# Performance work log

Hardware: AMD Instinct MI355X
Metric: run time of the kernel (lower is better)

The kernel has to match this reference:

```python
import jax, jax.numpy as jnp
import numpy as np

NUM_HEADS = 32
NUM_KV_HEADS = 8
HEAD_DIM = 96
ROPE_BASE = 10000.0


def setup_inputs() -> dict:
    key = jax.random.key(0)
    k1, k2, k3 = jax.random.split(key, 3)
    B, S, H = 2, 2048, 3072
    op_size = NUM_HEADS * HEAD_DIM + 2 * NUM_KV_HEADS * HEAD_DIM  # 4608
    hidden_states = jax.random.normal(k1, (B, S, H), dtype=jnp.float32)
    w_qkv = jax.random.normal(k2, (op_size, H), dtype=jnp.float32) * (H ** -0.5)
    w_o = jax.random.normal(k3, (H, H), dtype=jnp.float32) * (H ** -0.5)
    position_ids = jnp.broadcast_to(jnp.arange(S, dtype=jnp.int64), (B, S))
    return {"hidden_states": hidden_states, "position_ids": position_ids,
            "w_qkv": w_qkv, "w_o": w_o}


def _rotate_half(x):
    x1, x2 = jnp.split(x, 2, axis=-1)
    return jnp.concatenate((-x2, x1), axis=-1)


def reference(hidden_states, position_ids, w_qkv, w_o):
    B, S, H = hidden_states.shape
    nh, nkv, hd = NUM_HEADS, NUM_KV_HEADS, HEAD_DIM
    n_rep = nh // nkv

    # fused QKV projection (torch Linear: x @ W^T)
    qkv = jnp.einsum('bsh,oh->bso', hidden_states, w_qkv)
    q_pos = nh * hd
    q = qkv[..., :q_pos].reshape(B, S, nh, hd).transpose(0, 2, 1, 3)
    k = qkv[..., q_pos:q_pos + nkv * hd].reshape(B, S, nkv, hd).transpose(0, 2, 1, 3)
    v = qkv[..., q_pos + nkv * hd:].reshape(B, S, nkv, hd).transpose(0, 2, 1, 3)

    # rotary embedding (Phi3RotaryEmbedding, rope_scaling=None)
    inv_freq = 1.0 / (ROPE_BASE ** (jnp.arange(0, hd, 2, dtype=jnp.float32) / hd))
    freqs = position_ids.astype(jnp.float32)[:, :, None] * inv_freq[None, None, :]  # [B,S,hd/2]
    emb = jnp.concatenate((freqs, freqs), axis=-1)  # [B,S,hd]
    cos = jnp.cos(emb)[:, None, :, :]  # unsqueeze head dim
    sin = jnp.sin(emb)[:, None, :, :]
    q = q * cos + _rotate_half(q) * sin
    k = k * cos + _rotate_half(k) * sin

    # repeat_kv: (B, nkv, S, hd) -> (B, nh, S, hd)
    k = jnp.repeat(k, n_rep, axis=1)
    v = jnp.repeat(v, n_rep, axis=1)

    # causal SDPA
    scale = 1.0 / jnp.sqrt(jnp.float32(hd))
    scores = jnp.einsum('bhqd,bhkd->bhqk', q, k) * scale
    causal = jnp.tril(jnp.ones((S, S), dtype=bool))
    scores = jnp.where(causal[None, None], scores, jnp.finfo(scores.dtype).min)
    probs = jax.nn.softmax(scores, axis=-1)
    attn = jnp.einsum('bhqk,bhkd->bhqd', probs, v)  # [B,nh,S,hd]

    attn = attn.transpose(0, 2, 1, 3).reshape(B, S, nh * hd)
    return jnp.einsum('bsh,oh->bso', attn, w_o)
```

## Files before the change

kernel.cpp:

```cpp
#include <hip/hip_runtime.h>
#include <stdint.h>
#include <math.h>

#define B_   2
#define S_   2048
#define H_   3072
#define NH   32
#define NKV  8
#define HD   96
#define OPSZ 4608
#define MM   (B_*S_)

typedef __attribute__((ext_vector_type(8))) short short8;
typedef __attribute__((ext_vector_type(4))) float floatx4;

__device__ __forceinline__ short f2bf(float f) {
    union { float f; uint32_t u; } v; v.f = f;
    uint32_t r = v.u + 0x7fffu + ((v.u >> 16) & 1u);
    return (short)(r >> 16);
}
__device__ __forceinline__ float bf2f(short s) {
    union { uint32_t u; float f; } v; v.u = ((uint32_t)(uint16_t)s) << 16;
    return v.f;
}
__device__ __forceinline__ uint32_t pk_bf_trunc(float lo, float hi) {
    union { float f; uint32_t u; } a, b; a.f = lo; b.f = hi;
    return (a.u >> 16) | (b.u & 0xFFFF0000u);
}
__device__ __forceinline__ float fast_exp2(float x) {
    float r;
    asm volatile("v_exp_f32 %0, %1" : "=v"(r) : "v"(x));
    return r;
}
__device__ __forceinline__ float dpp_max16(float x) {
    union { float f; int i; } a, t;
    a.f = x;
    t.i = __builtin_amdgcn_update_dpp(0, a.i, 0x128, 0xF, 0xF, false); a.f = fmaxf(a.f, t.f);
    t.i = __builtin_amdgcn_update_dpp(0, a.i, 0x124, 0xF, 0xF, false); a.f = fmaxf(a.f, t.f);
    t.i = __builtin_amdgcn_update_dpp(0, a.i, 0x122, 0xF, 0xF, false); a.f = fmaxf(a.f, t.f);
    t.i = __builtin_amdgcn_update_dpp(0, a.i, 0x121, 0xF, 0xF, false); a.f = fmaxf(a.f, t.f);
    return a.f;
}

__device__ __forceinline__ void async_load16(const void* g, void* l) {
    __builtin_amdgcn_global_load_lds(
        (const __attribute__((address_space(1))) void*)g,
        (__attribute__((address_space(3))) void*)l, 16, 0, 0);
}

#define CN1 (MM * H_ / 4)
#define CN2 (OPSZ * H_ / 4)
#define CN3 (H_ * H_ / 4)
__global__ void cast3_f32_bf16(const float* __restrict__ s1, const float* __restrict__ s2,
                               const float* __restrict__ s3, short* __restrict__ d1,
                               short* __restrict__ d2, short* __restrict__ d3) {
    int gid = blockIdx.x * blockDim.x + threadIdx.x;
    int stride = gridDim.x * blockDim.x;
    for (int i = gid; i < CN1; i += stride) {
        float4 v = ((const float4*)s1)[i];
        short4 o; o.x = f2bf(v.x); o.y = f2bf(v.y); o.z = f2bf(v.z); o.w = f2bf(v.w);
        ((short4*)d1)[i] = o;
    }
    for (int i = gid; i < CN2; i += stride) {
        float4 v = ((const float4*)s2)[i];
        short4 o; o.x = f2bf(v.x); o.y = f2bf(v.y); o.z = f2bf(v.z); o.w = f2bf(v.w);
        ((short4*)d2)[i] = o;
    }
    for (int i = gid; i < CN3; i += stride) {
        float4 v = ((const float4*)s3)[i];
        short4 o; o.x = f2bf(v.x); o.y = f2bf(v.y); o.z = f2bf(v.z); o.w = f2bf(v.w);
        ((short4*)d3)[i] = o;
    }
}

template<int OUT_BF16>
__global__ __launch_bounds__(256) void gemm_bt(const short* __restrict__ A, const short* __restrict__ Bm,
                                               float* __restrict__ Cf, short* __restrict__ Cb,
                                               int M, int N, int K) {
    __shared__ short la[2][128 * 32];
    __shared__ short lb[2][128 * 32];
    const int tid  = threadIdx.x;
    const int wave = tid >> 6, lane = tid & 63;
    const int L15  = lane & 15, quad = lane >> 4;

    const int num_n = N >> 7;
    const int linear = blockIdx.x;
    const int group = linear / (8 * num_n);
    const int rem   = linear % (8 * num_n);
    const int m0 = (group * 8 + (rem & 7)) * 128;
    const int n0 = (rem >> 3) * 128;
    const int wm = (wave >> 1) * 64, wn = (wave & 1) * 64;

    const int drow = wave * 32 + (lane >> 2);
    const int dcol = (lane & 3) * 8;
    const short* ga0 = A  + (size_t)(m0 + drow) * K + dcol;
    const short* ga1 = A  + (size_t)(m0 + drow + 16) * K + dcol;
    const short* gb0 = Bm + (size_t)(n0 + drow) * K + dcol;
    const short* gb1 = Bm + (size_t)(n0 + drow + 16) * K + dcol;
    const int lo0 = (wave * 32) * 32, lo1 = (wave * 32 + 16) * 32;

    floatx4 acc[4][4];
    for (int i = 0; i < 4; i++)
        for (int j = 0; j < 4; j++)
            acc[i][j] = (floatx4){0.f, 0.f, 0.f, 0.f};

    auto stage = [&](int k0, int buf) {
        async_load16(ga0 + k0, &la[buf][lo0]);
        async_load16(ga1 + k0, &la[buf][lo1]);
        async_load16(gb0 + k0, &lb[buf][lo0]);
        async_load16(gb1 + k0, &lb[buf][lo1]);
    };

    stage(0, 0);
    const int nk = K >> 5;
    for (int t = 0; t < nk; t++) {
        const int c = t & 1;
        __syncthreads();
        if (t + 1 < nk) stage((t + 1) << 5, 1 - c);

        short8 af[4], bfr[4];
        #pragma unroll
        for (int i = 0; i < 4; i++)
            af[i] = *(const short8*)&la[c][(wm + i * 16 + L15) * 32 + quad * 8];
        #pragma unroll
        for (int j = 0; j < 4; j++)
            bfr[j] = *(const short8*)&lb[c][(wn + j * 16 + L15) * 32 + quad * 8];
        #pragma unroll
        for (int i = 0; i < 4; i++)
            #pragma unroll
            for (int j = 0; j < 4; j++)
                acc[i][j] = __builtin_amdgcn_mfma_f32_16x16x32_bf16(af[i], bfr[j], acc[i][j], 0, 0, 0);
    }

    #pragma unroll
    for (int i = 0; i < 4; i++)
        #pragma unroll
        for (int j = 0; j < 4; j++)
            #pragma unroll
            for (int r = 0; r < 4; r++) {
                int row = m0 + wm + i * 16 + quad * 4 + r;
                int col = n0 + wn + j * 16 + L15;
                float v = acc[i][j][r];
                if (OUT_BF16) Cb[(size_t)row * N + col] = f2bf(v);
                else          Cf[(size_t)row * N + col] = v;
            }
}

__global__ void rope_reorder(const short* __restrict__ qkv, const int* __restrict__ pos_ids,
                             short* __restrict__ Q, short* __restrict__ Kc) {
    const int total = B_ * S_ * (NH + NKV) * HD;
    int idx = blockIdx.x * blockDim.x + threadIdx.x;
    int stride = gridDim.x * blockDim.x;
    for (; idx < total; idx += stride) {
        int d = idx % HD;
        int row = idx / HD;
        int h_all = row % (NH + NKV);
        int sb = row / (NH + NKV);
        int s = sb % S_;
        int b = sb / S_;
        int base = (b * S_ + s) * OPSZ;
        int off = (h_all < NH) ? (h_all * HD + d) : (H_ + (h_all - NH) * HD + d);
        float x = bf2f(qkv[base + off]);
        int delta = (d < 48) ? 48 : -48;
        float x2 = bf2f(qkv[base + off + delta]);
        int fi = d % 48;
        float inv = exp2f((float)fi * -0.2768273412f);
        float theta = (float)pos_ids[b * S_ + s] * inv;
        float sn, cs;
        __sincosf(theta, &sn, &cs);
        float rot = (d < 48) ? -x2 : x2;
        float outv = x * cs + rot * sn;
        if (h_all < NH) {
            outv *= 0.14724438747f;
            Q[((size_t)(b * NH + h_all) * S_ + s) * HD + d] = f2bf(outv);
        } else {
            int kvh = h_all - NH;
            size_t kaddr = ((size_t)(b * NKV + kvh) * S_ + s) * 128
                         + (((d >> 3) + s) & 15) * 8 + (d & 7);
            Kc[kaddr] = f2bf(outv);
        }
    }
}

__global__ __launch_bounds__(256) void v_transpose(const short* __restrict__ qkv, short* __restrict__ Vt) {
    __shared__ short tile[64 * 104];
    int blk = blockIdx.x;
    int st  = blk & 31;
    int kvh = (blk >> 5) & 7;
    int b   = blk >> 8;
    int s0  = st * 64;
    int tid = threadIdx.x;
    #pragma unroll
    for (int i = 0; i < 3; i++) {
        int c = tid + i * 256;
        int row = c / 12, col8 = c % 12;
        *(short8*)&tile[row * 104 + col8 * 8] =
            *(const short8*)(qkv + (size_t)(b * S_ + s0 + row) * OPSZ + 3840 + kvh * HD + col8 * 8);
    }
    __syncthreads();
    #pragma unroll
    for (int i = 0; i < 3; i++) {
        int c = tid + i * 256;
        int d = c >> 3, col8 = c & 7;
        int chunk0 = (col8 - d) & 7;
        short8 v;
        #pragma unroll
        for (int j = 0; j < 8; j++) {
            int col0 = chunk0 * 8 + j;
            int n = ((col0 >> 5) << 1) | (col0 & 1);
            int t = (col0 & 31) >> 1;
            v[j] = tile[(n * 16 + t) * 104 + d];
        }
        *(short8*)(Vt + ((size_t)(b * NKV + kvh) * HD + d) * S_ + s0 + col8 * 8) = v;
    }
}

__global__ __launch_bounds__(256) void flash_attn(const short* __restrict__ Q, const short* __restrict__ Kc,
                                                  const short* __restrict__ Vt, short* __restrict__ attn) {
    __shared__ short kl[2][64 * 128];
    __shared__ short vl[2][112 * 64];
    __shared__ short pl[4][32 * 72];
    const int x = blockIdx.x, h = blockIdx.y, b = blockIdx.z;
    const int kvh = h >> 2;
    const int tid = threadIdx.x, wave = tid >> 6, lane = tid & 63;
    const int L15 = lane & 15, quad = lane >> 4;

    #pragma unroll
    for (int i = 0; i < 2; i++) {
        uint32_t* p = (uint32_t*)&vl[i][96 * 64];
        #pragma unroll
        for (int k = 0; k < 2; k++) {
            int idx = tid + k * 256;
            p[idx] = (idx < 32) ? 0x3F803F80u : 0u;
        }
    }

    const short* kbase = Kc + (size_t)(b * NKV + kvh) * S_ * 128;
    const short* vbase = Vt + (size_t)(b * NKV + kvh) * HD * S_;
    const int klane   = lane * 8;
    const int vrow_lo = lane >> 3;
    const int vcol    = (lane & 7) * 8;

    int rotK[3], rotV[2];
    #pragma unroll
    for (int kk = 0; kk < 3; kk++) rotK[kk] = ((kk * 4 + quad + L15) & 15) * 8;
    #pragma unroll
    for (int kk = 0; kk < 2; kk++) rotV[kk] = ((kk * 4 + quad + L15) & 7) * 8;

    auto stage = [&](int kv0, int buf) {
        const short* ksrc = kbase + (size_t)kv0 * 128;
        #pragma unroll
        for (int i = 0; i < 4; i++) {
            int ck = wave * 4 + i;
            async_load16(ksrc + ck * 512 + klane, &kl[buf][ck * 512]);
        }
        #pragma unroll
        for (int i = 0; i < 3; i++) {
            int ck = wave * 3 + i;
            async_load16(vbase + (size_t)(ck * 8 + vrow_lo) * S_ + kv0 + vcol, &vl[buf][ck * 512]);
        }
    };

    #pragma unroll
    for (int pp = 0; pp < 2; pp++) {
        const int qt = pp ? x : (15 - x);
        const int q0 = qt * 128;
        const int jmax = 2 * qt + 2;

        short8 qf[2][3];
        #pragma unroll
        for (int mm = 0; mm < 2; mm++) {
            const short* qrow = Q + ((size_t)(b * NH + h) * S_ + q0 + wave * 32 + mm * 16 + L15) * HD;
            #pragma unroll
            for (int kk = 0; kk < 3; kk++) qf[mm][kk] = *(const short8*)(qrow + kk * 32 + quad * 8);
        }
        floatx4 o[2][7];
        float m_r[2][4];
        #pragma unroll
        for (int mm = 0; mm < 2; mm++) {
            #pragma unroll
            for (int nn = 0; nn < 7; nn++) o[mm][nn] = (floatx4){0.f, 0.f, 0.f, 0.f};
            #pragma unroll
            for (int r = 0; r < 4; r++) m_r[mm][r] = -3.0e38f;
        }

        __syncthreads();
        stage(0, 0);

        for (int j = 0; j < jmax; j++) {
            const int c = j & 1;
            const int kv0 = j * 64;
            __syncthreads();
            if (j + 1 < jmax) stage(kv0 + 64, 1 - c);

            const short* klp = kl[c];
            const short* vlp = vl[c];

            floatx4 sacc[2][4];
            #pragma unroll
            for (int mm = 0; mm < 2; mm++)
                #pragma unroll
                for (int n = 0; n < 4; n++) sacc[mm][n] = (floatx4){0.f, 0.f, 0.f, 0.f};
            #pragma unroll
            for (int n = 0; n < 4; n++)
                #pragma unroll
                for (int kk = 0; kk < 3; kk++) {
                    short8 kf = *(const short8*)&klp[(n * 16 + L15) * 128 + rotK[kk]];
                    sacc[0][n] = __builtin_amdgcn_mfma_f32_16x16x32_bf16(qf[0][kk], kf, sacc[0][n], 0, 0, 0);
                    sacc[1][n] = __builtin_amdgcn_mfma_f32_16x16x32_bf16(qf[1][kk], kf, sacc[1][n], 0, 0, 0);
                }

            #pragma unroll
            for (int mm = 0; mm < 2; mm++) {
                const int tbase = q0 + wave * 32 + mm * 16;
                if (kv0 + 63 > tbase) {
                    int qr_base = tbase + quad * 4;
                    #pragma unroll
                    for (int n = 0; n < 4; n++) {
                        int kv = kv0 + n * 16 + L15;
                        #pragma unroll
                        for (int r = 0; r < 4; r++)
                            if (kv > qr_base + r) sacc[mm][n][r] = -3.0e38f;
                    }
                }
                float alpha[4];
                #pragma unroll
                for (int r = 0; r < 4; r++) {
                    float mx = fmaxf(fmaxf(sacc[mm][0][r], sacc[mm][1][r]),
                                     fmaxf(sacc[mm][2][r], sacc[mm][3][r]));
                    mx = dpp_max16(mx);
                    float mn = fmaxf(m_r[mm][r], mx);
                    alpha[r] = fast_exp2(m_r[mm][r] - mn);
                    m_r[mm][r] = mn;
                }
                #pragma unroll
                for (int n = 0; n < 4; n++)
                    #pragma unroll
                    for (int r = 0; r < 4; r++)
                        sacc[mm][n][r] = fast_exp2(sacc[mm][n][r] - m_r[mm][r]);
                #pragma unroll
                for (int r = 0; r < 4; r++) {
                    int prow = mm * 16 + quad * 4 + r;
                    *(uint32_t*)&pl[wave][prow * 72 + 2 * L15]      = pk_bf_trunc(sacc[mm][0][r], sacc[mm][1][r]);
                    *(uint32_t*)&pl[wave][prow * 72 + 32 + 2 * L15] = pk_bf_trunc(sacc[mm][2][r], sacc[mm][3][r]);
                }
                #pragma unroll
                for (int nn = 0; nn < 7; nn++)
                    #pragma unroll
                    for (int r = 0; r < 4; r++) o[mm][nn][r] *= alpha[r];
            }

            #pragma unroll
            for (int kk = 0; kk < 2; kk++) {
                short8 af0 = *(const short8*)&pl[wave][L15 * 72 + kk * 32 + quad * 8];
                short8 af1 = *(const short8*)&pl[wave][(16 + L15) * 72 + kk * 32 + quad * 8];
                #pragma unroll
                for (int nn = 0; nn < 7; nn++) {
                    short8 vf = *(const short8*)&vlp[(nn * 16 + L15) * 64 + rotV[kk]];
                    o[0][nn] = __builtin_amdgcn_mfma_f32_16x16x32_bf16(af0, vf, o[0][nn], 0, 0, 0);
                    o[1][nn] = __builtin_amdgcn_mfma_f32_16x16x32_bf16(af1, vf, o[1][nn], 0, 0, 0);
                }
            }
        }

        #pragma unroll
        for (int mm = 0; mm < 2; mm++) {
            float inv_l[4];
            #pragma unroll
            for (int r = 0; r < 4; r++) {
                float l = __shfl(o[mm][6][r], lane & 48);
                inv_l[r] = 1.0f / l;
            }
            #pragma unroll
            for (int nn = 0; nn < 6; nn++)
                #pragma unroll
                for (int r = 0; r < 4; r++) {
                    float v = o[mm][nn][r] * inv_l[r];
                    int row = q0 + wave * 32 + mm * 16 + quad * 4 + r;
                    attn[((size_t)(b * S_) + row) * H_ + h * HD + nn * 16 + L15] = f2bf(v);
                }
        }
    }
}

extern "C" void kernel_launch(void* const* d_in, const int* in_sizes, int n_in,
                              void* d_out, int out_size, void* d_ws, size_t ws_size,
                              hipStream_t stream) {
    const float* hid  = (const float*)d_in[0];
    const int*   pos  = (const int*)d_in[1];
    const float* wqkv = (const float*)d_in[2];
    const float* wo   = (const float*)d_in[3];
    float* out = (float*)d_out;
    char* ws = (char*)d_ws;

    short* hid_b  = (short*)(ws + 0L);
    short* wqkv_b = (short*)(ws + 25165824L);
    short* wo_b   = (short*)(ws + 53477376L);
    short* qkv_b  = (short*)(ws + 72351744L);
    short* q_b    = (short*)(ws + 110100480L);
    short* k_b    = (short*)(ws + 135266304L);
    short* vt_b   = (short*)(ws + 143654912L);
    short* attn_b = (short*)(ws + 0L);

    cast3_f32_bf16<<<4096, 256, 0, stream>>>(hid, wqkv, wo, hid_b, wqkv_b, wo_b);

    gemm_bt<1><<<(OPSZ / 128) * (MM / 128), 256, 0, stream>>>(hid_b, wqkv_b, nullptr, qkv_b, MM, OPSZ, H_);

    rope_reorder<<<8192, 256, 0, stream>>>(qkv_b, pos, q_b, k_b);
    v_transpose<<<512, 256, 0, stream>>>(qkv_b, vt_b);

    flash_attn<<<dim3(8, NH, B_), 256, 0, stream>>>(q_b, k_b, vt_b, attn_b);

    gemm_bt<0><<<(H_ / 128) * (MM / 128), 256, 0, stream>>>(attn_b, wo_b, out, nullptr, MM, H_, H_);
}
```

Before: 565.9 us.

## Replace GEMM with 256x256-tile, 8-wave kernel with swizzled LDS and XCD remap

Replaces the 128x128, 4-wave bf16 GEMM with a 256x256-tile, 512-thread kernel that uses a K step of 64 and 128KB of LDS. Global-to-LDS prefetch is double buffered and kept two tiles ahead, the LDS layout uses an XOR swizzle to avoid bank conflicts, and block ids are remapped across the 8 XCDs. MFMA phases are interleaved with staged loads using barriers and setprio. The goal is more data reuse per tile and better overlap of memory and compute in both projection GEMMs. In exchange, register pressure is high (128 accumulator floats per lane) and the grid is smaller, which could leave CUs underfilled: 4608/256 x 16 = 288 blocks for the QKV GEMM and 192 for the output GEMM. The wrapped nx index also issues redundant loads at the tail.

```diff
diff --git a/kernel.cpp b/kernel.cpp
--- a/kernel.cpp
+++ b/kernel.cpp
@@ -74,73 +74,147 @@
 }
 
 template<int OUT_BF16>
-__global__ __launch_bounds__(256) void gemm_bt(const short* __restrict__ A, const short* __restrict__ Bm,
-                                               float* __restrict__ Cf, short* __restrict__ Cb,
-                                               int M, int N, int K) {
-    __shared__ short la[2][128 * 32];
-    __shared__ short lb[2][128 * 32];
-    const int tid  = threadIdx.x;
-    const int wave = tid >> 6, lane = tid & 63;
-    const int L15  = lane & 15, quad = lane >> 4;
-
-    const int num_n = N >> 7;
-    const int linear = blockIdx.x;
-    const int group = linear / (8 * num_n);
-    const int rem   = linear % (8 * num_n);
-    const int m0 = (group * 8 + (rem & 7)) * 128;
-    const int n0 = (rem >> 3) * 128;
-    const int wm = (wave >> 1) * 64, wn = (wave & 1) * 64;
-
-    const int drow = wave * 32 + (lane >> 2);
-    const int dcol = (lane & 3) * 8;
-    const short* ga0 = A  + (size_t)(m0 + drow) * K + dcol;
-    const short* ga1 = A  + (size_t)(m0 + drow + 16) * K + dcol;
-    const short* gb0 = Bm + (size_t)(n0 + drow) * K + dcol;
-    const short* gb1 = Bm + (size_t)(n0 + drow + 16) * K + dcol;
-    const int lo0 = (wave * 32) * 32, lo1 = (wave * 32 + 16) * 32;
-
-    floatx4 acc[4][4];
-    for (int i = 0; i < 4; i++)
+__global__ __launch_bounds__(512, 2) void gemm256(const short* __restrict__ A, const short* __restrict__ Bm,
+                                                  float* __restrict__ Cf, short* __restrict__ Cb,
+                                                  int M, int N, int K) {
+    __shared__ __align__(16) char smem[131072];
+    const int tid = threadIdx.x;
+    const int w = tid >> 6, l = tid & 63;
+    const int L15 = l & 15, quad = l >> 4;
+
+    const int gm = M >> 8;
+    const int nwg = gridDim.x;
+    const int id = blockIdx.x;
+    const int qq = nwg >> 3, rr = nwg & 7;
+    const int xcd = id & 7, sidx = id >> 3;
+    const int wgid = (xcd < rr ? xcd * (qq + 1) : rr * (qq + 1) + (xcd - rr) * qq) + sidx;
+    const int m0 = (wgid % gm) << 8;
+    const int n0 = (wgid / gm) << 8;
+    const int wm = (w >> 2) << 7;
+    const int wn = (w & 3) << 6;
+
+    const int cbl = ((l & 3) * 16) ^ (((l >> 5) & 1) << 5);
+    uint32_t aofs[4], bofs[4];
+    #pragma unroll
+    for (int j = 0; j < 4; j++) {
+        const int s = j * 8 + w;
+        const int row = ((s >> 1) << 4) + (l >> 2);
+        const int colb = ((s & 1) << 6) + cbl;
+        aofs[j] = (uint32_t)(m0 + row) * (uint32_t)(K * 2) + colb;
+        bofs[j] = (uint32_t)(n0 + row) * (uint32_t)(K * 2) + colb;
+    }
+    char* ldsA = (char*)smem;
+    char* ldsB = (char*)smem + 65536;
+    const int dstw = w * 1024;
+
+    const int lane_off = L15 * 64 + ((quad * 16) ^ (((L15 >> 3) & 1) << 5));
+    const int aoff = (w >> 2) * 16384 + lane_off;
+    const int boff = (w & 3) * 8192 + lane_off;
+
+    floatx4 acc[8][4];
+    #pragma unroll
+    for (int i = 0; i < 8; i++)
+        #pragma unroll
         for (int j = 0; j < 4; j++)
             acc[i][j] = (floatx4){0.f, 0.f, 0.f, 0.f};
 
-    auto stage = [&](int k0, int buf) {
-        async_load16(ga0 + k0, &la[buf][lo0]);
-        async_load16(ga1 + k0, &la[buf][lo1]);
-        async_load16(gb0 + k0, &lb[buf][lo0]);
-        async_load16(gb1 + k0, &lb[buf][lo1]);
+    auto stageA = [&](int kt, int buf) {
+        const uint32_t kb = (uint32_t)kt << 7;
+        #pragma unroll
+        for (int j = 0; j < 4; j++)
+            async_load16((const char*)A + (size_t)(aofs[j] + kb), ldsA + buf * 32768 + j * 8192 + dstw);
     };
-
-    stage(0, 0);
-    const int nk = K >> 5;
-    for (int t = 0; t < nk; t++) {
+    auto stageB = [&](int kt, int buf) {
+        const uint32_t kb = (uint32_t)kt << 7;
+        #pragma unroll
+        for (int j = 0; j < 4; j++)
+            async_load16((const char*)Bm + (size_t)(bofs[j] + kb), ldsB + buf * 32768 + j * 8192 + dstw);
+    };
+
+    const int nkt = K >> 6;
+    stageB(0, 0); stageA(0, 0);
+    stageB(1, 1); stageA(1, 1);
+
+    for (int t = 0; t < nkt; t++) {
         const int c = t & 1;
-        __syncthreads();
-        if (t + 1 < nk) stage((t + 1) << 5, 1 - c);
-
-        short8 af[4], bfr[4];
+        const char* ab = ldsA + c * 32768 + aoff;
+        const char* bb = ldsB + c * 32768 + boff;
+        int nx = t + 2; if (nx >= nkt) nx -= nkt;
+
+        asm volatile("s_waitcnt vmcnt(8)" ::: "memory");
+        __builtin_amdgcn_s_barrier();
+        __builtin_amdgcn_sched_barrier(0);
+
+        short8 a0[4][2], a1[4][2], bfrag[4][2];
         #pragma unroll
         for (int i = 0; i < 4; i++)
-            af[i] = *(const short8*)&la[c][(wm + i * 16 + L15) * 32 + quad * 8];
+            #pragma unroll
+            for (int kk = 0; kk < 2; kk++)
+                a0[i][kk] = *(const short8*)(ab + i * 2048 + kk * 1024);
         #pragma unroll
         for (int j = 0; j < 4; j++)
-            bfr[j] = *(const short8*)&lb[c][(wn + j * 16 + L15) * 32 + quad * 8];
+            #pragma unroll
+            for (int kk = 0; kk < 2; kk++)
+                bfrag[j][kk] = *(const short8*)(bb + j * 2048 + kk * 1024);
+        __builtin_amdgcn_s_barrier();
+        __builtin_amdgcn_s_setprio(1);
+        #pragma unroll
+        for (int kk = 0; kk < 2; kk++)
+            #pragma unroll
+            for (int i = 0; i < 4; i++)
+                #pragma unroll
+                for (int j = 0; j < 2; j++)
+                    acc[i][j] = __builtin_amdgcn_mfma_f32_16x16x32_bf16(a0[i][kk], bfrag[j][kk], acc[i][j], 0, 0, 0);
+        __builtin_amdgcn_s_setprio(0);
+        __builtin_amdgcn_s_barrier();
+        __builtin_amdgcn_s_setprio(1);
+        #pragma unroll
+        for (int kk = 0; kk < 2; kk++)
+            #pragma unroll
+            for (int i = 0; i < 4; i++)
+                #pragma unroll
+                for (int j = 2; j < 4; j++)
+                    acc[i][j] = __builtin_amdgcn_mfma_f32_16x16x32_bf16(a0[i][kk], bfrag[j][kk], acc[i][j], 0, 0, 0);
+        __builtin_amdgcn_s_setprio(0);
         #pragma unroll
         for (int i = 0; i < 4; i++)
             #pragma unroll
-            for (int j = 0; j < 4; j++)
-                acc[i][j] = __builtin_amdgcn_mfma_f32_16x16x32_bf16(af[i], bfr[j], acc[i][j], 0, 0, 0);
-    }
-
-    #pragma unroll
-    for (int i = 0; i < 4; i++)
+            for (int kk = 0; kk < 2; kk++)
+                a1[i][kk] = *(const short8*)(ab + 8192 + i * 2048 + kk * 1024);
+        __builtin_amdgcn_s_barrier();
+        stageB(nx, c);
+        __builtin_amdgcn_s_setprio(1);
+        #pragma unroll
+        for (int kk = 0; kk < 2; kk++)
+            #pragma unroll
+            for (int i = 0; i < 4; i++)
+                #pragma unroll
+                for (int j = 0; j < 2; j++)
+                    acc[4 + i][j] = __builtin_amdgcn_mfma_f32_16x16x32_bf16(a1[i][kk], bfrag[j][kk], acc[4 + i][j], 0, 0, 0);
+        __builtin_amdgcn_s_setprio(0);
+        __builtin_amdgcn_s_barrier();
+        stageA(nx, c);
+        __builtin_amdgcn_s_setprio(1);
+        #pragma unroll
+        for (int kk = 0; kk < 2; kk++)
+            #pragma unroll
+            for (int i = 0; i < 4; i++)
+                #pragma unroll
+                for (int j = 2; j < 4; j++)
+                    acc[4 + i][j] = __builtin_amdgcn_mfma_f32_16x16x32_bf16(a1[i][kk], bfrag[j][kk], acc[4 + i][j], 0, 0, 0);
+        __builtin_amdgcn_s_setprio(0);
+    }
+    asm volatile("s_waitcnt vmcnt(0)" ::: "memory");
+
+    #pragma unroll
+    for (int i = 0; i < 8; i++)
         #pragma unroll
         for (int j = 0; j < 4; j++)
             #pragma unroll
             for (int r = 0; r < 4; r++) {
-                int row = m0 + wm + i * 16 + quad * 4 + r;
-                int col = n0 + wn + j * 16 + L15;
-                float v = acc[i][j][r];
+                const int row = m0 + wm + i * 16 + quad * 4 + r;
+                const int col = n0 + wn + j * 16 + L15;
+                const float v = acc[i][j][r];
                 if (OUT_BF16) Cb[(size_t)row * N + col] = f2bf(v);
                 else          Cf[(size_t)row * N + col] = v;
             }
@@ -404,12 +478,12 @@
 
     cast3_f32_bf16<<<4096, 256, 0, stream>>>(hid, wqkv, wo, hid_b, wqkv_b, wo_b);
 
-    gemm_bt<1><<<(OPSZ / 128) * (MM / 128), 256, 0, stream>>>(hid_b, wqkv_b, nullptr, qkv_b, MM, OPSZ, H_);
+    gemm256<1><<<(OPSZ / 256) * (MM / 256), 512, 0, stream>>>(hid_b, wqkv_b, nullptr, qkv_b, MM, OPSZ, H_);
 
     rope_reorder<<<8192, 256, 0, stream>>>(qkv_b, pos, q_b, k_b);
     v_transpose<<<512, 256, 0, stream>>>(qkv_b, vt_b);
 
     flash_attn<<<dim3(8, NH, B_), 256, 0, stream>>>(q_b, k_b, vt_b, attn_b);
 
-    gemm_bt<0><<<(H_ / 128) * (MM / 128), 256, 0, stream>>>(attn_b, wo_b, out, nullptr, MM, H_, H_);
-}
+    gemm256<0><<<(H_ / 256) * (MM / 256), 512, 0, stream>>>(attn_b, wo_b, out, nullptr, MM, H_, H_);
+}
```

New measurement: 552.1 us. 2.4% less time.
